# Performance work log

Hardware: AMD Instinct MI355X
Metric: run time of the kernel (lower is better)

The kernel has to match this reference:

```python
import jax, jax.numpy as jnp
import numpy as np

N_NODES = 50000
N_EDGES = 1600000
DIM = 128
EDGE_DIM = 16
IN_DIM = 2 * DIM + EDGE_DIM


def setup_inputs() -> dict:
    key = jax.random.key(0)
    ks = jax.random.split(key, 8)
    h = jax.random.normal(ks[0], (N_NODES, DIM), dtype=jnp.float32)
    src = jax.random.randint(ks[1], (N_EDGES,), 0, N_NODES)
    dst = jax.random.randint(ks[2], (N_EDGES,), 0, N_NODES)
    edge_attr = jax.random.normal(ks[3], (N_EDGES, EDGE_DIM), dtype=jnp.float32)
    # Linear weights stored as [in, out] so x @ W + b
    W1 = jax.random.normal(ks[4], (IN_DIM, DIM), dtype=jnp.float32) / np.sqrt(IN_DIM)
    b1 = jnp.zeros((DIM,), dtype=jnp.float32)
    W2 = jax.random.normal(ks[5], (DIM, DIM), dtype=jnp.float32) / np.sqrt(DIM)
    b2 = jnp.zeros((DIM,), dtype=jnp.float32)
    gamma = jnp.ones((DIM,), dtype=jnp.float32)
    beta = jnp.zeros((DIM,), dtype=jnp.float32)
    return {"h": h, "src": src, "dst": dst, "edge_attr": edge_attr,
            "W1": W1, "b1": b1, "W2": W2, "b2": b2, "gamma": gamma, "beta": beta}


def _layer_norm(x, gamma, beta, eps=1e-5):
    mu = jnp.mean(x, axis=-1, keepdims=True)
    var = jnp.mean(jnp.square(x - mu), axis=-1, keepdims=True)
    return (x - mu) * jax.lax.rsqrt(var + eps) * gamma + beta


def reference(h, src, dst, edge_attr, W1, b1, W2, b2, gamma, beta):
    # gather endpoint features + edge attrs -> [E, 2*dim+edge_dim]
    x = jnp.concatenate([h[src], h[dst], edge_attr], axis=-1)
    hdn = jax.nn.gelu(x @ W1 + b1, approximate=False)  # torch nn.GELU default is exact
    messages = hdn @ W2 + b2                           # [E, dim]
    # scatter-add messages to destination nodes
    agg = jax.ops.segment_sum(messages, dst, num_segments=h.shape[0])
    return _layer_norm(h + agg, gamma, beta)
```

## Files before the change

### kernel.cpp

```cpp
#include <hip/hip_runtime.h>
#include <math.h>

#define NUM_NODES 50000
#define NUM_EDGES 1600000
#define DIM 128
#define EDGE_DIM 16
#define NKT1 18
#define NKT2 8
#define MT 64
#define CSTRIDE 132
#define NSCAN 196
#define NODE_BLOCKS ((NUM_NODES + 63) / 64)

typedef short bf16x8 __attribute__((ext_vector_type(8)));
typedef float floatx16 __attribute__((ext_vector_type(16)));
typedef unsigned short ushort4v __attribute__((ext_vector_type(4)));
typedef unsigned short ushort8v __attribute__((ext_vector_type(8)));

__device__ __forceinline__ unsigned short f2b(float f) {
    unsigned u = __builtin_bit_cast(unsigned, f);
    u += 0x7FFFu + ((u >> 16) & 1u);
    return (unsigned short)(u >> 16);
}

__global__ void prep_kernel(const float* __restrict__ W1, const float* __restrict__ W2,
                            short* __restrict__ W1f, short* __restrict__ W2f)
{
    int gid = blockIdx.x * 256 + threadIdx.x;
    if (gid < NKT1 * 4 * 64) {
        int lane = gid & 63, nb = (gid >> 6) & 3, kt = gid >> 8;
        int n = nb * 32 + (lane & 31);
        int kbase = kt * 16 + (lane >> 5) * 8;
        #pragma unroll
        for (int j = 0; j < 8; ++j) {
            int k = kbase + j;
            W1f[gid * 8 + j] = (k < 272) ? (short)f2b(W1[(size_t)k * DIM + n]) : (short)0;
        }
    } else if (gid < NKT1 * 4 * 64 + NKT2 * 4 * 64) {
        int g2 = gid - NKT1 * 4 * 64;
        int lane = g2 & 63, nb = (g2 >> 6) & 3, kt = g2 >> 8;
        int n = nb * 32 + (lane & 31);
        int kbase = kt * 16 + (lane >> 5) * 8;
        #pragma unroll
        for (int j = 0; j < 8; ++j)
            W2f[g2 * 8 + j] = (short)f2b(W2[(size_t)(kbase + j) * DIM + n]);
    }
}

__global__ void hconv_kernel(const float* __restrict__ h, unsigned short* __restrict__ h_bf) {
    int t = blockIdx.x * 256 + threadIdx.x;
    float4 v = ((const float4*)h)[t];
    ushort4v o;
    o.x = f2b(v.x); o.y = f2b(v.y); o.z = f2b(v.z); o.w = f2b(v.w);
    ((ushort4v*)h_bf)[t] = o;
}

__global__ void hist_kernel(const int* __restrict__ dst, int* __restrict__ counts) {
    int e = blockIdx.x * 256 + threadIdx.x;
    atomicAdd(&counts[dst[e]], 1);
}

__global__ void scanA_kernel(const int* __restrict__ counts, int* __restrict__ bsum) {
    __shared__ int sb[256];
    int t = threadIdx.x, i = blockIdx.x * 256 + t;
    int v = (i < NUM_NODES) ? counts[i] : 0;
    sb[t] = v; __syncthreads();
    for (int off = 1; off < 256; off <<= 1) {
        int x = (t >= off) ? sb[t - off] : 0;
        __syncthreads(); sb[t] += x; __syncthreads();
    }
    if (t == 255) bsum[blockIdx.x] = sb[255];
}

__global__ void scanB_kernel(const int* __restrict__ bsum, int* __restrict__ boffs) {
    __shared__ int sb[256];
    int t = threadIdx.x;
    int v = (t < NSCAN) ? bsum[t] : 0;
    sb[t] = v; __syncthreads();
    for (int off = 1; off < 256; off <<= 1) {
        int x = (t >= off) ? sb[t - off] : 0;
        __syncthreads(); sb[t] += x; __syncthreads();
    }
    if (t < NSCAN) boffs[t] = sb[t] - v;
}

__global__ void scanC_kernel(const int* __restrict__ counts, const int* __restrict__ boffs,
                             int* __restrict__ cursor) {
    __shared__ int sb[256];
    int t = threadIdx.x, i = blockIdx.x * 256 + t;
    int v = (i < NUM_NODES) ? counts[i] : 0;
    sb[t] = v; __syncthreads();
    for (int off = 1; off < 256; off <<= 1) {
        int x = (t >= off) ? sb[t - off] : 0;
        __syncthreads(); sb[t] += x; __syncthreads();
    }
    if (i < NUM_NODES) cursor[i] = boffs[blockIdx.x] + sb[t] - v;
}

__global__ void scatter3_kernel(const int* __restrict__ src, const int* __restrict__ dst,
                                int* __restrict__ cursor, int* __restrict__ src_s,
                                int* __restrict__ dst_s, int* __restrict__ eid_s)
{
    int e = blockIdx.x * 256 + threadIdx.x;
    int d = dst[e];
    int p = atomicAdd(&cursor[d], 1);
    src_s[p] = src[e];
    dst_s[p] = d;
    eid_s[p] = e;
}

__global__ __launch_bounds__(256, 4) void edge_kernel(
    const unsigned short* __restrict__ h_bf,
    const int* __restrict__ src_s, const int* __restrict__ dst_s,
    const int* __restrict__ eid_s, const float* __restrict__ ea,
    const short* __restrict__ W1f, const float* __restrict__ pb1,
    float* __restrict__ aggh)
{
    __shared__ __align__(16) short xbuf[36 * 64 * 8];
    __shared__ int srcl[MT], dstl[MT], eidl[MT];
    float* cbuf = (float*)xbuf;

    const int tid = threadIdx.x;
    const long long base = (long long)blockIdx.x * MT;

    if (tid < MT)            srcl[tid]          = src_s[base + tid];
    else if (tid < 2 * MT)   dstl[tid - MT]     = dst_s[base + tid - MT];
    else if (tid < 3 * MT)   eidl[tid - 2 * MT] = eid_s[base + tid - 2 * MT];
    __syncthreads();

    #pragma unroll
    for (int it = 0; it < 8; ++it) {
        int g = it * 256 + tid;
        int kt2 = g >> 6, row = g & 63;
        int node = (kt2 < 16) ? srcl[row] : dstl[row];
        ushort8v v = *(const ushort8v*)(h_bf + (size_t)node * DIM + (kt2 & 15) * 8);
        *(ushort8v*)&xbuf[(kt2 * 64 + row) * 8] = v;
    }
    {
        int row = (tid & 127) >> 1, hc = tid & 1;
        if (tid < 128) {
            const float4* er = (const float4*)(ea + (size_t)eidl[row] * EDGE_DIM + hc * 8);
            float4 v0 = er[0], v1 = er[1];
            ushort8v o;
            o[0] = f2b(v0.x); o[1] = f2b(v0.y); o[2] = f2b(v0.z); o[3] = f2b(v0.w);
            o[4] = f2b(v1.x); o[5] = f2b(v1.y); o[6] = f2b(v1.z); o[7] = f2b(v1.w);
            *(ushort8v*)&xbuf[((32 + hc) * 64 + row) * 8] = o;
        } else {
            ushort8v z = {0, 0, 0, 0, 0, 0, 0, 0};
            *(ushort8v*)&xbuf[((34 + hc) * 64 + row) * 8] = z;
        }
    }
    __syncthreads();

    const int lane = tid & 63, wave = tid >> 6;
    const int lm = lane & 31, half = lane >> 5;

    floatx16 acc0 = {}, acc1 = {};
    #pragma unroll
    for (int kt = 0; kt < NKT1; ++kt) {
        bf16x8 a0 = *(const bf16x8*)&xbuf[((kt * 2 + half) * 64 + lm) * 8];
        bf16x8 a1 = *(const bf16x8*)&xbuf[((kt * 2 + half) * 64 + 32 + lm) * 8];
        bf16x8 b  = *(const bf16x8*)(W1f + ((kt * 4 + wave) * 64 + lane) * 8);
        acc0 = __builtin_amdgcn_mfma_f32_32x32x16_bf16(a0, b, acc0, 0, 0, 0);
        acc1 = __builtin_amdgcn_mfma_f32_32x32x16_bf16(a1, b, acc1, 0, 0, 0);
    }
    __syncthreads();

    float bb = pb1[wave * 32 + lm];
    #pragma unroll
    for (int s = 0; s < 2; ++s) {
        const floatx16& A = s ? acc1 : acc0;
        #pragma unroll
        for (int r = 0; r < 16; ++r) {
            int rr = (r & 3) + 8 * (r >> 2) + 4 * half;
            float v = A[r] + bb;
            float u = v * (1.5957691216f + 0.0713548163f * v * v);
            u = fminf(u, 80.f);
            float t = __expf(u);
            float g = v * t * __builtin_amdgcn_rcpf(t + 1.f);
            cbuf[(s * 32 + rr) * CSTRIDE + wave * 32 + lm] = g;
        }
    }
    __syncthreads();

    {
        int col = tid & 127, hf = tid >> 7;
        int r0 = hf * 32, r1 = r0 + 32;
        float s = 0.f;
        int cur = dstl[r0];
        for (int r = r0; r < r1; ++r) {
            s += cbuf[r * CSTRIDE + col];
            int nxt = (r == r1 - 1) ? -1 : dstl[r + 1];
            if (nxt != cur) {
                atomicAdd(&aggh[(size_t)cur * DIM + col], s);
                s = 0.f;
                cur = nxt;
            }
        }
    }
}

__global__ __launch_bounds__(256, 4) void node_ln_kernel(
    const float* __restrict__ aggh, const int* __restrict__ counts,
    const short* __restrict__ W2f, const float* __restrict__ pb2,
    const float* __restrict__ h, const float* __restrict__ gamma,
    const float* __restrict__ beta, float* __restrict__ out)
{
    __shared__ __align__(16) float sbuf[64 * CSTRIDE];
    __shared__ int cntl[64];
    short* abuf = (short*)sbuf;

    const int tid = threadIdx.x;
    const int n0 = blockIdx.x * 64;

    if (tid < 64) {
        int node = n0 + tid;
        cntl[tid] = (node < NUM_NODES) ? counts[node] : 0;
    }
    #pragma unroll
    for (int it = 0; it < 4; ++it) {
        int g = it * 256 + tid;
        int kt2 = g >> 6, row = g & 63;
        int node = n0 + row;
        ushort8v o = {0, 0, 0, 0, 0, 0, 0, 0};
        if (node < NUM_NODES) {
            const float4* p = (const float4*)(aggh + (size_t)node * DIM + kt2 * 8);
            float4 v0 = p[0], v1 = p[1];
            o[0] = f2b(v0.x); o[1] = f2b(v0.y); o[2] = f2b(v0.z); o[3] = f2b(v0.w);
            o[4] = f2b(v1.x); o[5] = f2b(v1.y); o[6] = f2b(v1.z); o[7] = f2b(v1.w);
        }
        *(ushort8v*)&abuf[(kt2 * 64 + row) * 8] = o;
    }
    __syncthreads();

    const int lane = tid & 63, wave = tid >> 6;
    const int lm = lane & 31, half = lane >> 5;

    floatx16 acc0 = {}, acc1 = {};
    #pragma unroll
    for (int kt = 0; kt < NKT2; ++kt) {
        bf16x8 a0 = *(const bf16x8*)&abuf[((kt * 2 + half) * 64 + lm) * 8];
        bf16x8 a1 = *(const bf16x8*)&abuf[((kt * 2 + half) * 64 + 32 + lm) * 8];
        bf16x8 b  = *(const bf16x8*)(W2f + ((kt * 4 + wave) * 64 + lane) * 8);
        acc0 = __builtin_amdgcn_mfma_f32_32x32x16_bf16(a0, b, acc0, 0, 0, 0);
        acc1 = __builtin_amdgcn_mfma_f32_32x32x16_bf16(a1, b, acc1, 0, 0, 0);
    }
    __syncthreads();

    float bb2 = pb2[wave * 32 + lm];
    #pragma unroll
    for (int s = 0; s < 2; ++s) {
        const floatx16& A = s ? acc1 : acc0;
        #pragma unroll
        for (int r = 0; r < 16; ++r) {
            int rr = (r & 3) + 8 * (r >> 2) + 4 * half;
            int row = s * 32 + rr;
            sbuf[row * CSTRIDE + wave * 32 + lm] = A[r] + (float)cntl[row] * bb2;
        }
    }
    __syncthreads();

    {
        int row = tid >> 2, q = tid & 3;
        int node = n0 + row;
        if (node < NUM_NODES) {
            float4 xv[8];
            float s = 0.f, ss = 0.f;
            const float4* hp = (const float4*)(h + (size_t)node * DIM + q * 32);
            #pragma unroll
            for (int i = 0; i < 8; ++i) {
                float4 c = *(const float4*)&sbuf[row * CSTRIDE + q * 32 + i * 4];
                float4 hh = hp[i];
                float4 x;
                x.x = c.x + hh.x; x.y = c.y + hh.y; x.z = c.z + hh.z; x.w = c.w + hh.w;
                xv[i] = x;
                s  += x.x + x.y + x.z + x.w;
                ss += x.x * x.x + x.y * x.y + x.z * x.z + x.w * x.w;
            }
            s  += __shfl_xor(s, 1, 64);  s  += __shfl_xor(s, 2, 64);
            ss += __shfl_xor(ss, 1, 64); ss += __shfl_xor(ss, 2, 64);
            float mu = s * (1.f / DIM);
            float var = ss * (1.f / DIM) - mu * mu;
            float rs = rsqrtf(var + 1e-5f);
            const float4* gp = (const float4*)(gamma + q * 32);
            const float4* bp = (const float4*)(beta + q * 32);
            float4* op = (float4*)(out + (size_t)node * DIM + q * 32);
            #pragma unroll
            for (int i = 0; i < 8; ++i) {
                float4 g4 = gp[i], b4 = bp[i], o;
                o.x = (xv[i].x - mu) * rs * g4.x + b4.x;
                o.y = (xv[i].y - mu) * rs * g4.y + b4.y;
                o.z = (xv[i].z - mu) * rs * g4.z + b4.z;
                o.w = (xv[i].w - mu) * rs * g4.w + b4.w;
                op[i] = o;
            }
        }
    }
}

extern "C" void kernel_launch(void* const* d_in, const int* in_sizes, int n_in,
                              void* d_out, int out_size, void* d_ws, size_t ws_size,
                              hipStream_t stream)
{
    const float* h     = (const float*)d_in[0];
    const int*   src   = (const int*)d_in[1];
    const int*   dst   = (const int*)d_in[2];
    const float* ea    = (const float*)d_in[3];
    const float* W1    = (const float*)d_in[4];
    const float* pb1   = (const float*)d_in[5];
    const float* W2    = (const float*)d_in[6];
    const float* pb2   = (const float*)d_in[7];
    const float* gamma = (const float*)d_in[8];
    const float* beta  = (const float*)d_in[9];
    float* out = (float*)d_out;

    char* ws = (char*)d_ws;
    short* W1f   = (short*)ws;
    short* W2f   = (short*)(ws + 73728);
    int* counts  = (int*)(ws + 106496);
    int* cursor  = (int*)(ws + 306496);
    int* bsum    = (int*)(ws + 506496);
    int* boffs   = (int*)(ws + 507520);
    int* src_s   = (int*)(ws + 508544);
    int* dst_s   = (int*)(ws + 6908544);
    int* eid_s   = (int*)(ws + 13308544);
    unsigned short* h_bf = (unsigned short*)(ws + 19708544);
    float* aggh  = (float*)(ws + 32508544);

    hipMemsetAsync(aggh, 0, (size_t)NUM_NODES * DIM * sizeof(float), stream);
    hipMemsetAsync(counts, 0, NUM_NODES * sizeof(int), stream);

    prep_kernel<<<26, 256, 0, stream>>>(W1, W2, W1f, W2f);
    hconv_kernel<<<6250, 256, 0, stream>>>(h, h_bf);
    hist_kernel<<<NUM_EDGES / 256, 256, 0, stream>>>(dst, counts);
    scanA_kernel<<<NSCAN, 256, 0, stream>>>(counts, bsum);
    scanB_kernel<<<1, 256, 0, stream>>>(bsum, boffs);
    scanC_kernel<<<NSCAN, 256, 0, stream>>>(counts, boffs, cursor);
    scatter3_kernel<<<NUM_EDGES / 256, 256, 0, stream>>>(src, dst, cursor,
                                                         src_s, dst_s, eid_s);
    edge_kernel<<<NUM_EDGES / MT, 256, 0, stream>>>(h_bf, src_s, dst_s, eid_s, ea,
                                                    W1f, pb1, aggh);
    node_ln_kernel<<<NODE_BLOCKS, 256, 0, stream>>>(aggh, counts, W2f, pb2,
                                                    h, gamma, beta, out);
}
```

Before: 619.0 us.

## Fuse setup kernels, pack src/eid pairs, restructure edge gather and segmented reduce

Merges weight prep, h-to-bf16 conversion and the dst histogram into one launch. The scatter now writes src and edge id as a packed int2. The edge kernel gathers rows directly from per-lane registers, without staging indices in shared memory or an extra barrier. The segmented reduce now has each thread sum 8 rows over 4 columns with float4 LDS reads, which may issue more atomics than the old 32-row runs.

Measured after the change: 942.7 us. 52.3% more time.

```diff
diff --git a/kernel.cpp b/kernel.cpp
--- a/kernel.cpp
+++ b/kernel.cpp
@@ -23,41 +23,42 @@
     return (unsigned short)(u >> 16);
 }
 
-__global__ void prep_kernel(const float* __restrict__ W1, const float* __restrict__ W2,
-                            short* __restrict__ W1f, short* __restrict__ W2f)
-{
-    int gid = blockIdx.x * 256 + threadIdx.x;
-    if (gid < NKT1 * 4 * 64) {
-        int lane = gid & 63, nb = (gid >> 6) & 3, kt = gid >> 8;
-        int n = nb * 32 + (lane & 31);
-        int kbase = kt * 16 + (lane >> 5) * 8;
-        #pragma unroll
-        for (int j = 0; j < 8; ++j) {
-            int k = kbase + j;
-            W1f[gid * 8 + j] = (k < 272) ? (short)f2b(W1[(size_t)k * DIM + n]) : (short)0;
-        }
-    } else if (gid < NKT1 * 4 * 64 + NKT2 * 4 * 64) {
-        int g2 = gid - NKT1 * 4 * 64;
-        int lane = g2 & 63, nb = (g2 >> 6) & 3, kt = g2 >> 8;
-        int n = nb * 32 + (lane & 31);
-        int kbase = kt * 16 + (lane >> 5) * 8;
-        #pragma unroll
-        for (int j = 0; j < 8; ++j)
-            W2f[g2 * 8 + j] = (short)f2b(W2[(size_t)(kbase + j) * DIM + n]);
-    }
-}
-
-__global__ void hconv_kernel(const float* __restrict__ h, unsigned short* __restrict__ h_bf) {
-    int t = blockIdx.x * 256 + threadIdx.x;
-    float4 v = ((const float4*)h)[t];
-    ushort4v o;
-    o.x = f2b(v.x); o.y = f2b(v.y); o.z = f2b(v.z); o.w = f2b(v.w);
-    ((ushort4v*)h_bf)[t] = o;
-}
-
-__global__ void hist_kernel(const int* __restrict__ dst, int* __restrict__ counts) {
-    int e = blockIdx.x * 256 + threadIdx.x;
-    atomicAdd(&counts[dst[e]], 1);
+__global__ void setup_kernel(const float* __restrict__ W1, const float* __restrict__ W2,
+                             short* __restrict__ W1f, short* __restrict__ W2f,
+                             const float* __restrict__ h, unsigned short* __restrict__ h_bf,
+                             const int* __restrict__ dst, int* __restrict__ counts)
+{
+    int b = blockIdx.x, tid = threadIdx.x;
+    if (b < 26) {
+        int gid = b * 256 + tid;
+        if (gid < NKT1 * 4 * 64) {
+            int lane = gid & 63, nb = (gid >> 6) & 3, kt = gid >> 8;
+            int n = nb * 32 + (lane & 31);
+            int kbase = kt * 16 + (lane >> 5) * 8;
+            #pragma unroll
+            for (int j = 0; j < 8; ++j) {
+                int k = kbase + j;
+                W1f[gid * 8 + j] = (k < 272) ? (short)f2b(W1[(size_t)k * DIM + n]) : (short)0;
+            }
+        } else if (gid < NKT1 * 4 * 64 + NKT2 * 4 * 64) {
+            int g2 = gid - NKT1 * 4 * 64;
+            int lane = g2 & 63, nb = (g2 >> 6) & 3, kt = g2 >> 8;
+            int n = nb * 32 + (lane & 31);
+            int kbase = kt * 16 + (lane >> 5) * 8;
+            #pragma unroll
+            for (int j = 0; j < 8; ++j)
+                W2f[g2 * 8 + j] = (short)f2b(W2[(size_t)(kbase + j) * DIM + n]);
+        }
+    } else if (b < 6276) {
+        int t = (b - 26) * 256 + tid;
+        float4 v = ((const float4*)h)[t];
+        ushort4v o;
+        o.x = f2b(v.x); o.y = f2b(v.y); o.z = f2b(v.z); o.w = f2b(v.w);
+        ((ushort4v*)h_bf)[t] = o;
+    } else {
+        int e = (b - 6276) * 256 + tid;
+        atomicAdd(&counts[dst[e]], 1);
+    }
 }
 
 __global__ void scanA_kernel(const int* __restrict__ counts, int* __restrict__ bsum) {
@@ -97,62 +98,67 @@
     if (i < NUM_NODES) cursor[i] = boffs[blockIdx.x] + sb[t] - v;
 }
 
-__global__ void scatter3_kernel(const int* __restrict__ src, const int* __restrict__ dst,
-                                int* __restrict__ cursor, int* __restrict__ src_s,
-                                int* __restrict__ dst_s, int* __restrict__ eid_s)
+__global__ void scatter_kernel(const int* __restrict__ src, const int* __restrict__ dst,
+                               int* __restrict__ cursor, int2* __restrict__ se_s,
+                               int* __restrict__ dst_s)
 {
     int e = blockIdx.x * 256 + threadIdx.x;
     int d = dst[e];
     int p = atomicAdd(&cursor[d], 1);
-    src_s[p] = src[e];
+    se_s[p] = make_int2(src[e], e);
     dst_s[p] = d;
-    eid_s[p] = e;
 }
 
 __global__ __launch_bounds__(256, 4) void edge_kernel(
     const unsigned short* __restrict__ h_bf,
-    const int* __restrict__ src_s, const int* __restrict__ dst_s,
-    const int* __restrict__ eid_s, const float* __restrict__ ea,
+    const int2* __restrict__ se_s, const int* __restrict__ dst_s,
+    const float* __restrict__ ea,
     const short* __restrict__ W1f, const float* __restrict__ pb1,
     float* __restrict__ aggh)
 {
     __shared__ __align__(16) short xbuf[36 * 64 * 8];
-    __shared__ int srcl[MT], dstl[MT], eidl[MT];
+    __shared__ int dstl[MT];
     float* cbuf = (float*)xbuf;
 
     const int tid = threadIdx.x;
+    const int lane = tid & 63, wave = tid >> 6;
     const long long base = (long long)blockIdx.x * MT;
 
-    if (tid < MT)            srcl[tid]          = src_s[base + tid];
-    else if (tid < 2 * MT)   dstl[tid - MT]     = dst_s[base + tid - MT];
-    else if (tid < 3 * MT)   eidl[tid - 2 * MT] = eid_s[base + tid - 2 * MT];
-    __syncthreads();
-
-    #pragma unroll
-    for (int it = 0; it < 8; ++it) {
-        int g = it * 256 + tid;
-        int kt2 = g >> 6, row = g & 63;
-        int node = (kt2 < 16) ? srcl[row] : dstl[row];
-        ushort8v v = *(const ushort8v*)(h_bf + (size_t)node * DIM + (kt2 & 15) * 8);
-        *(ushort8v*)&xbuf[(kt2 * 64 + row) * 8] = v;
-    }
     {
-        int row = (tid & 127) >> 1, hc = tid & 1;
+        int row = lane;
+        int2 se = se_s[base + row];
+        int dn  = dst_s[base + row];
+        if (tid < MT) dstl[tid] = dn;
+        const ushort8v* hs = (const ushort8v*)(h_bf + (size_t)se.x * DIM);
+        const ushort8v* hd = (const ushort8v*)(h_bf + (size_t)dn * DIM);
+        #pragma unroll
+        for (int it = 0; it < 4; ++it) {
+            int kt2 = it * 4 + wave;
+            *(ushort8v*)&xbuf[(kt2 * 64 + row) * 8] = hs[kt2];
+        }
+        #pragma unroll
+        for (int it = 0; it < 4; ++it) {
+            int kt2 = it * 4 + wave;
+            *(ushort8v*)&xbuf[((16 + kt2) * 64 + row) * 8] = hd[kt2];
+        }
         if (tid < 128) {
-            const float4* er = (const float4*)(ea + (size_t)eidl[row] * EDGE_DIM + hc * 8);
+            int r2 = tid >> 1, hc = tid & 1;
+            int eid = se_s[base + r2].y;
+            const float4* er = (const float4*)(ea + (size_t)eid * EDGE_DIM + hc * 8);
             float4 v0 = er[0], v1 = er[1];
             ushort8v o;
             o[0] = f2b(v0.x); o[1] = f2b(v0.y); o[2] = f2b(v0.z); o[3] = f2b(v0.w);
             o[4] = f2b(v1.x); o[5] = f2b(v1.y); o[6] = f2b(v1.z); o[7] = f2b(v1.w);
-            *(ushort8v*)&xbuf[((32 + hc) * 64 + row) * 8] = o;
+            *(ushort8v*)&xbuf[((32 + hc) * 64 + r2) * 8] = o;
         } else {
+            int t2 = tid - 128;
+            int r2 = t2 >> 1, hc = t2 & 1;
             ushort8v z = {0, 0, 0, 0, 0, 0, 0, 0};
-            *(ushort8v*)&xbuf[((34 + hc) * 64 + row) * 8] = z;
-        }
-    }
-    __syncthreads();
-
-    const int lane = tid & 63, wave = tid >> 6;
+            *(ushort8v*)&xbuf[((34 + hc) * 64 + r2) * 8] = z;
+        }
+    }
+    __syncthreads();
+
     const int lm = lane & 31, half = lane >> 5;
 
     floatx16 acc0 = {}, acc1 = {};
@@ -166,34 +172,46 @@
     }
     __syncthreads();
 
-    float bb = pb1[wave * 32 + lm];
-    #pragma unroll
-    for (int s = 0; s < 2; ++s) {
-        const floatx16& A = s ? acc1 : acc0;
-        #pragma unroll
-        for (int r = 0; r < 16; ++r) {
-            int rr = (r & 3) + 8 * (r >> 2) + 4 * half;
-            float v = A[r] + bb;
-            float u = v * (1.5957691216f + 0.0713548163f * v * v);
-            u = fminf(u, 80.f);
-            float t = __expf(u);
-            float g = v * t * __builtin_amdgcn_rcpf(t + 1.f);
-            cbuf[(s * 32 + rr) * CSTRIDE + wave * 32 + lm] = g;
-        }
-    }
-    __syncthreads();
-
     {
-        int col = tid & 127, hf = tid >> 7;
-        int r0 = hf * 32, r1 = r0 + 32;
-        float s = 0.f;
-        int cur = dstl[r0];
-        for (int r = r0; r < r1; ++r) {
-            s += cbuf[r * CSTRIDE + col];
-            int nxt = (r == r1 - 1) ? -1 : dstl[r + 1];
+        float bb = pb1[wave * 32 + lm];
+        #pragma unroll
+        for (int s = 0; s < 2; ++s) {
+            const floatx16& A = s ? acc1 : acc0;
+            #pragma unroll
+            for (int r = 0; r < 16; ++r) {
+                int rr = (r & 3) + 8 * (r >> 2) + 4 * half;
+                float v = A[r] + bb;
+                float u = v * (1.5957691216f + 0.0713548163f * v * v);
+                u = fminf(u, 80.f);
+                float t = __expf(u);
+                float g = v * t * __builtin_amdgcn_rcpf(t + 1.f);
+                cbuf[(s * 32 + rr) * CSTRIDE + wave * 32 + lm] = g;
+            }
+        }
+    }
+    __syncthreads();
+
+    {
+        int q = tid & 31, g = tid >> 5;
+        int r0 = g * 8;
+        float4 v[8];
+        #pragma unroll
+        for (int r = 0; r < 8; ++r)
+            v[r] = *(const float4*)&cbuf[(r0 + r) * CSTRIDE + q * 4];
+        int d[8];
+        #pragma unroll
+        for (int r = 0; r < 8; ++r) d[r] = dstl[r0 + r];
+        float4 s = make_float4(0.f, 0.f, 0.f, 0.f);
+        int cur = d[0];
+        #pragma unroll
+        for (int r = 0; r < 8; ++r) {
+            s.x += v[r].x; s.y += v[r].y; s.z += v[r].z; s.w += v[r].w;
+            int nxt = (r == 7) ? -1 : d[r + 1];
             if (nxt != cur) {
-                atomicAdd(&aggh[(size_t)cur * DIM + col], s);
-                s = 0.f;
+                float* ap = &aggh[(size_t)cur * DIM + q * 4];
+                atomicAdd(ap + 0, s.x); atomicAdd(ap + 1, s.y);
+                atomicAdd(ap + 2, s.z); atomicAdd(ap + 3, s.w);
+                s = make_float4(0.f, 0.f, 0.f, 0.f);
                 cur = nxt;
             }
         }
@@ -321,25 +339,20 @@
     int* cursor  = (int*)(ws + 306496);
     int* bsum    = (int*)(ws + 506496);
     int* boffs   = (int*)(ws + 507520);
-    int* src_s   = (int*)(ws + 508544);
-    int* dst_s   = (int*)(ws + 6908544);
-    int* eid_s   = (int*)(ws + 13308544);
+    int2* se_s   = (int2*)(ws + 508544);
+    int* dst_s   = (int*)(ws + 13308544);
     unsigned short* h_bf = (unsigned short*)(ws + 19708544);
     float* aggh  = (float*)(ws + 32508544);
 
+    hipMemsetAsync(counts, 0, NUM_NODES * sizeof(int), stream);
     hipMemsetAsync(aggh, 0, (size_t)NUM_NODES * DIM * sizeof(float), stream);
-    hipMemsetAsync(counts, 0, NUM_NODES * sizeof(int), stream);
-
-    prep_kernel<<<26, 256, 0, stream>>>(W1, W2, W1f, W2f);
-    hconv_kernel<<<6250, 256, 0, stream>>>(h, h_bf);
-    hist_kernel<<<NUM_EDGES / 256, 256, 0, stream>>>(dst, counts);
+
+    setup_kernel<<<12526, 256, 0, stream>>>(W1, W2, W1f, W2f, h, h_bf, dst, counts);
     scanA_kernel<<<NSCAN, 256, 0, stream>>>(counts, bsum);
     scanB_kernel<<<1, 256, 0, stream>>>(bsum, boffs);
     scanC_kernel<<<NSCAN, 256, 0, stream>>>(counts, boffs, cursor);
-    scatter3_kernel<<<NUM_EDGES / 256, 256, 0, stream>>>(src, dst, cursor,
-                                                         src_s, dst_s, eid_s);
-    edge_kernel<<<NUM_EDGES / MT, 256, 0, stream>>>(h_bf, src_s, dst_s, eid_s, ea,
-                                                    W1f, pb1, aggh);
+    scatter_kernel<<<NUM_EDGES / 256, 256, 0, stream>>>(src, dst, cursor, se_s, dst_s);
+    edge_kernel<<<NUM_EDGES / MT, 256, 0, stream>>>(h_bf, se_s, dst_s, ea, W1f, pb1, aggh);
     node_ln_kernel<<<NODE_BLOCKS, 256, 0, stream>>>(aggh, counts, W2f, pb2,
                                                     h, gamma, beta, out);
 }
```
